# Kernel tuning notes

Measured on AMD Instinct MI355X. Metric: run time of the kernel, lower is better.

The kernel has to match this reference:

```python
import jax, jax.numpy as jnp
import numpy as np
import math

D_MODEL = 1024
NUM_HEADS = 16
D_K = D_MODEL // NUM_HEADS
THETA = 10000.0
B, T = 2, 2048


def _trunc_normal(key, shape, std):
    # truncated normal in [-3std, 3std]
    return jax.random.truncated_normal(key, -3.0, 3.0, shape, jnp.float32) * std


def setup_inputs() -> dict:
    key = jax.random.key(0)
    ks = jax.random.split(key, 6)
    sigma = math.sqrt(2.0 / (D_MODEL + D_MODEL))
    x = jax.random.normal(ks[0], (B, T, D_MODEL), jnp.float32)
    Wq = _trunc_normal(ks[1], (D_MODEL, D_MODEL), sigma)  # [out, in]
    Wk = _trunc_normal(ks[2], (D_MODEL, D_MODEL), sigma)
    Wv = _trunc_normal(ks[3], (D_MODEL, D_MODEL), sigma)
    Wo = _trunc_normal(ks[4], (D_MODEL, D_MODEL), sigma)
    token_positions = jnp.arange(T, dtype=jnp.int64 if jax.config.read('jax_enable_x64') else jnp.int32)
    return {"x": x, "Wq": Wq, "Wk": Wk, "Wv": Wv, "Wo": Wo,
            "token_positions": token_positions}


def _rotate_half(x):
    x0 = x[..., ::2]
    x1 = x[..., 1::2]
    return jnp.stack((-x1, x0), axis=-1).reshape(x.shape)


def _rope(x, token_positions):
    # x: [B, H, T, d_k]; token_positions: [T]
    inv_freq = 1.0 / (THETA ** (jnp.arange(0, D_K, 2, dtype=jnp.float32) / D_K))
    ang = token_positions.astype(jnp.float32)[:, None] * inv_freq  # [T, d_k/2]
    cos = jnp.repeat(jnp.cos(ang), 2, axis=-1)  # [T, d_k]
    sin = jnp.repeat(jnp.sin(ang), 2, axis=-1)
    xdtype = x.dtype
    xf = x.astype(jnp.float32)
    return (xf * cos + _rotate_half(xf) * sin).astype(xdtype)


def reference(x, Wq, Wk, Wv, Wo, token_positions):
    b, t, _ = x.shape

    def proj_split(W):
        h = jnp.einsum('btd,od->bto', x, W)
        return h.reshape(b, t, NUM_HEADS, D_K).transpose(0, 2, 1, 3)  # [B,H,T,d_k]

    Q = _rope(proj_split(Wq), token_positions)
    K = _rope(proj_split(Wk), token_positions)
    V = proj_split(Wv)

    scores = jnp.einsum('bhqd,bhkd->bhqk', Q, K) / math.sqrt(D_K)
    causal = jnp.tril(jnp.ones((t, t), dtype=bool))  # [T,T]
    scores = jnp.where(causal, scores, -jnp.inf)
    weights = jax.nn.softmax(scores, axis=-1)
    attn = jnp.einsum('bhqk,bhkd->bhqd', weights, V)  # [B,H,T,d_v]
    merged = attn.transpose(0, 2, 1, 3).reshape(b, t, D_MODEL)
    return jnp.einsum('btd,od->bto', merged, Wo)
```

## Files before the change

kernel.cpp:

```cpp
#include <hip/hip_runtime.h>
#include <cstdint>
#include <cstddef>

#define DMODEL 1024
#define NHEADS 16
#define DKH    64
#define SEQT   2048
#define NBATCH 2
#define MTOT   (NBATCH*SEQT)

#define QSCALE 0.1803368801111204f

using h16   = _Float16;
using h16x2 = __attribute__((ext_vector_type(2))) h16;
using h16x4 = __attribute__((ext_vector_type(4))) h16;
using h16x8 = __attribute__((ext_vector_type(8))) h16;
using f32x4 = __attribute__((ext_vector_type(4))) float;
using fp16x2_native = __attribute__((ext_vector_type(2))) __fp16;

using as1_void = __attribute__((address_space(1))) void;
using as3_void = __attribute__((address_space(3))) void;

__device__ __forceinline__ void gll16(void* lds, const void* g) {
  __builtin_amdgcn_global_load_lds((const as1_void*)g, (as3_void*)lds, 16, 0, 0);
}

__device__ __forceinline__ h16x2 pkrtz(float a, float b) {
  fp16x2_native t = __builtin_amdgcn_cvt_pkrtz(a, b);
  h16x2 r; r[0] = (h16)t[0]; r[1] = (h16)t[1]; return r;
}

__device__ __forceinline__ h16x4 cvt4(const float4 v) {
  h16x4 o; o[0] = (h16)v.x; o[1] = (h16)v.y; o[2] = (h16)v.z; o[3] = (h16)v.w; return o;
}

__global__ void prep_kernel(const float4* __restrict__ x,
                            const float4* __restrict__ Wq, const float4* __restrict__ Wk,
                            const float4* __restrict__ Wv, const float4* __restrict__ Wo,
                            h16x4* __restrict__ xb,
                            h16x4* __restrict__ wqb, h16x4* __restrict__ wkb,
                            h16x4* __restrict__ wvb, h16x4* __restrict__ wob,
                            float* __restrict__ ctab, float* __restrict__ stab) {
  const int tid  = blockIdx.x * blockDim.x + threadIdx.x;
  const int nthr = gridDim.x * blockDim.x;
  const int NX4 = MTOT * DMODEL / 4;
  const int NW4 = DMODEL * DMODEL / 4;
  for (int i = tid; i < NX4; i += nthr) xb[i] = cvt4(x[i]);
  for (int i = tid; i < NW4; i += nthr) {
    wqb[i] = cvt4(Wq[i]);
    wkb[i] = cvt4(Wk[i]);
    wvb[i] = cvt4(Wv[i]);
    wob[i] = cvt4(Wo[i]);
  }
  for (int i = tid; i < SEQT * 32; i += nthr) {
    const int t = i >> 5, fi = i & 31;
    float inv = __expf(-0.28782313662425575f * (float)fi);
    float ang = (float)t * inv;
    float s, c;
    sincosf(ang, &s, &c);
    ctab[i] = c; stab[i] = s;
  }
}

__device__ __forceinline__ void gemm128_bt(const h16* __restrict__ A, const h16* __restrict__ Bt,
                                           int m0, int n0, h16* Al, h16* Bl, f32x4 acc[4][4]) {
  const int tid  = threadIdx.x;
  const int lane = tid & 63;
  const int wv   = tid >> 6;
  const int wm = (wv >> 1) * 64, wn = (wv & 1) * 64;
  const int lr = lane & 15, lk = (lane >> 4) * 8;
  const int srow = tid >> 2, scol = (tid & 3) * 8;
  const h16* a0 = A  + (size_t)(m0 + srow) * DMODEL + scol;
  const h16* a1 = a0 + (size_t)64 * DMODEL;
  const h16* b0 = Bt + (size_t)(n0 + srow) * DMODEL + scol;
  const h16* b1 = b0 + (size_t)64 * DMODEL;
  h16* alds0 = Al + wv * 512;
  h16* alds1 = Al + 2048 + wv * 512;
  h16* blds0 = Bl + wv * 512;
  h16* blds1 = Bl + 2048 + wv * 512;

  for (int k0 = 0; k0 < DMODEL; k0 += 32) {
    __syncthreads();
    gll16(alds0, a0 + k0);
    gll16(alds1, a1 + k0);
    gll16(blds0, b0 + k0);
    gll16(blds1, b1 + k0);
    __syncthreads();
    h16x8 af[4], bfr[4];
#pragma unroll
    for (int i = 0; i < 4; ++i) {
      af[i]  = *(const h16x8*)(Al + (wm + i * 16 + lr) * 32 + lk);
      bfr[i] = *(const h16x8*)(Bl + (wn + i * 16 + lr) * 32 + lk);
    }
#pragma unroll
    for (int i = 0; i < 4; ++i)
#pragma unroll
      for (int j = 0; j < 4; ++j)
        acc[i][j] = __builtin_amdgcn_mfma_f32_16x16x32_f16(af[i], bfr[j], acc[i][j], 0, 0, 0);
  }
}

__global__ __launch_bounds__(256, 2) void qkv_kernel(
    const h16* __restrict__ xb,
    const h16* __restrict__ wqb, const h16* __restrict__ wkb, const h16* __restrict__ wvb,
    const float* __restrict__ ctab, const float* __restrict__ stab,
    h16* __restrict__ Qb, h16* __restrict__ Kb, h16* __restrict__ Vt) {
  __shared__ h16 Al[128 * 32], Bl[128 * 32];
  const int which = blockIdx.z;
  const h16* W = (which == 0) ? wqb : (which == 1) ? wkb : wvb;
  const int m0 = blockIdx.x * 128, n0 = blockIdx.y * 128;
  f32x4 acc[4][4];
  const f32x4 zero4 = {0.f, 0.f, 0.f, 0.f};
#pragma unroll
  for (int i = 0; i < 4; ++i)
#pragma unroll
    for (int j = 0; j < 4; ++j) acc[i][j] = zero4;

  gemm128_bt(xb, W, m0, n0, Al, Bl, acc);

  const int lane = threadIdx.x & 63, wv = threadIdx.x >> 6;
  const int wm = (wv >> 1) * 64, wn = (wv & 1) * 64;
  const int lr4 = ((lane >> 4) << 2), lc = lane & 15;
  if (which == 2) {
#pragma unroll
    for (int i = 0; i < 4; ++i) {
      const int m = m0 + wm + i * 16 + lr4;
      const int b = m >> 11, t = m & (SEQT - 1);
#pragma unroll
      for (int j = 0; j < 4; ++j) {
        const int n = n0 + wn + j * 16 + lc;
        const int h = n >> 6, d = n & 63;
        h16x4 o4;
#pragma unroll
        for (int r = 0; r < 4; ++r) o4[r] = (h16)acc[i][j][r];
        *(h16x4*)&Vt[((size_t)(b * NHEADS + h) * DKH + d) * SEQT + t] = o4;
      }
    }
  } else {
#pragma unroll
    for (int i = 0; i < 4; ++i) {
#pragma unroll
      for (int j = 0; j < 4; ++j) {
        const int n = n0 + wn + j * 16 + lc;
        const int h = n >> 6, d = n & 63;
#pragma unroll
        for (int r = 0; r < 4; ++r) {
          const int m = m0 + wm + i * 16 + lr4 + r;
          const int b = m >> 11, t = m & (SEQT - 1);
          float v = acc[i][j][r];
          float pv = __shfl_xor(v, 1);
          const int fi = d >> 1;
          float c = ctab[t * 32 + fi], s = stab[t * 32 + fi];
          float res = (d & 1) ? (v * c + pv * s) : (v * c - pv * s);
          if (which == 0) res *= QSCALE;
          h16* dst = (which == 0) ? Qb : Kb;
          dst[((size_t)(b * NHEADS + h) * SEQT + t) * DKH + d] = (h16)res;
        }
      }
    }
  }
}

__global__ __launch_bounds__(256, 4) void attn_kernel(
    const h16* __restrict__ Qb, const h16* __restrict__ Kb,
    const h16* __restrict__ Vt, h16* __restrict__ Mg) {
  __shared__ h16 Kl[128][76];
  __shared__ h16 Vl[64][140];
  const int linear = blockIdx.x + 32 * blockIdx.y;
  const int v   = linear & 7;
  const int p   = linear >> 3;
  const int w   = p >> 5;
  const int c32 = p & 31;
  const int u   = (c32 + w) & 3;
  const int bh  = c32;
  const int qt  = (u == 0) ? v : (u == 1) ? (15 - v) : (u == 2) ? (16 + v) : (31 - v);
  const int b = bh >> 4, h = bh & 15;
  const int tid = threadIdx.x, lane = tid & 63, wv = tid >> 6;
  const int lr = lane & 15, lg = lane >> 4;
  const int q0 = qt * 64;
  const int qbase = q0 + wv * 16;
  const int q = qbase + lr;
  const h16* Qp = Qb + ((size_t)bh * SEQT + qbase) * DKH;
  const h16* Kp = Kb + (size_t)bh * SEQT * DKH;
  const h16* Vp = Vt + (size_t)bh * DKH * SEQT;

  h16x8 qf[2];
#pragma unroll
  for (int kk = 0; kk < 2; ++kk)
    qf[kk] = *(const h16x8*)(Qp + lr * DKH + kk * 32 + lg * 8);

  float mrow = -3.0e38f, lsum = 0.f;
  f32x4 o[4];
  const f32x4 zero4 = {0.f, 0.f, 0.f, 0.f};
#pragma unroll
  for (int di = 0; di < 4; ++di) o[di] = zero4;

  const int sr = tid >> 2, sc = (tid & 3) * 16;
  const int nkt = (qt >> 1) + 1;
  for (int kt = 0; kt < nkt; ++kt) {
    const int k0 = kt * 128;
    __syncthreads();
#pragma unroll
    for (int half = 0; half < 2; ++half) {
      const int r = half * 64 + sr;
      *(uint4*)&Kl[r][sc]     = *(const uint4*)(Kp + (size_t)(k0 + r) * DKH + sc);
      *(uint4*)&Kl[r][sc + 8] = *(const uint4*)(Kp + (size_t)(k0 + r) * DKH + sc + 8);
    }
#pragma unroll
    for (int half = 0; half < 2; ++half) {
      const int c = half * 64 + sc;
      *(uint4*)&Vl[sr][c]     = *(const uint4*)(Vp + (size_t)sr * SEQT + k0 + c);
      *(uint4*)&Vl[sr][c + 8] = *(const uint4*)(Vp + (size_t)sr * SEQT + k0 + c + 8);
    }
    __syncthreads();

    f32x4 s[8];
    __builtin_amdgcn_s_setprio(1);
#pragma unroll
    for (int ni = 0; ni < 8; ++ni) {
      s[ni] = zero4;
#pragma unroll
      for (int kk = 0; kk < 2; ++kk) {
        h16x8 kf = *(const h16x8*)&Kl[ni * 16 + lr][kk * 32 + lg * 8];
        s[ni] = __builtin_amdgcn_mfma_f32_16x16x32_f16(kf, qf[kk], s[ni], 0, 0, 0);
      }
    }
    __builtin_amdgcn_s_setprio(0);

    if (kt == nkt - 1) {
#pragma unroll
      for (int ni = 0; ni < 8; ++ni)
#pragma unroll
        for (int r = 0; r < 4; ++r) {
          const int key = k0 + ni * 16 + lg * 4 + r;
          if (key > q) s[ni][r] = -3.0e38f;
        }
    }

    float mx = s[0][0];
#pragma unroll
    for (int ni = 0; ni < 8; ++ni)
#pragma unroll
      for (int r = 0; r < 4; ++r) mx = fmaxf(mx, s[ni][r]);
    mx = fmaxf(mx, __shfl_xor(mx, 16));
    mx = fmaxf(mx, __shfl_xor(mx, 32));
    if (mx > mrow + 11.0f) {
      const float mnew = fmaxf(mrow, mx);
      const float scl = exp2f(mrow - mnew);
      mrow = mnew;
      lsum *= scl;
#pragma unroll
      for (int di = 0; di < 4; ++di)
#pragma unroll
        for (int r = 0; r < 4; ++r) o[di][r] *= scl;
    }
    float rs = 0.f;
#pragma unroll
    for (int ni = 0; ni < 8; ++ni)
#pragma unroll
      for (int r = 0; r < 4; ++r) {
        float p2 = exp2f(s[ni][r] - mrow);
        s[ni][r] = p2;
        rs += p2;
      }
    rs += __shfl_xor(rs, 16);
    rs += __shfl_xor(rs, 32);
    lsum += rs;

    __builtin_amdgcn_s_setprio(1);
#pragma unroll
    for (int ni = 0; ni < 8; ++ni) {
      h16x2 plo = pkrtz(s[ni][0], s[ni][1]);
      h16x2 phi = pkrtz(s[ni][2], s[ni][3]);
      h16x4 pb; pb[0] = plo[0]; pb[1] = plo[1]; pb[2] = phi[0]; pb[3] = phi[1];
#pragma unroll
      for (int di = 0; di < 4; ++di) {
        h16x4 va = *(const h16x4*)&Vl[di * 16 + lr][ni * 16 + lg * 4];
        o[di] = __builtin_amdgcn_mfma_f32_16x16x16f16(va, pb, o[di], 0, 0, 0);
      }
    }
    __builtin_amdgcn_s_setprio(0);
  }

  __syncthreads();
  const float inv = 1.0f / lsum;
#pragma unroll
  for (int di = 0; di < 4; ++di) {
    h16x2 lo = pkrtz(o[di][0] * inv, o[di][1] * inv);
    h16x2 hi = pkrtz(o[di][2] * inv, o[di][3] * inv);
    h16x4 o4; o4[0] = lo[0]; o4[1] = lo[1]; o4[2] = hi[0]; o4[3] = hi[1];
    *(h16x4*)&Kl[wv * 16 + lr][di * 16 + lg * 4] = o4;
  }
  __syncthreads();
  {
    const int row = tid >> 2, c0 = (tid & 3) * 16;
    h16* dst = Mg + ((size_t)(b * SEQT + q0 + row)) * DMODEL + h * DKH + c0;
    *(uint4*)dst       = *(const uint4*)&Kl[row][c0];
    *(uint4*)(dst + 8) = *(const uint4*)&Kl[row][c0 + 8];
  }
}

__global__ __launch_bounds__(256, 2) void proj_kernel(
    const h16* __restrict__ Mg, const h16* __restrict__ wob, float* __restrict__ out) {
  __shared__ h16 Al[128 * 32], Bl[128 * 32];
  const int m0 = blockIdx.x * 128, n0 = blockIdx.y * 128;
  f32x4 acc[4][4];
  const f32x4 zero4 = {0.f, 0.f, 0.f, 0.f};
#pragma unroll
  for (int i = 0; i < 4; ++i)
#pragma unroll
    for (int j = 0; j < 4; ++j) acc[i][j] = zero4;

  gemm128_bt(Mg, wob, m0, n0, Al, Bl, acc);

  const int lane = threadIdx.x & 63, wv = threadIdx.x >> 6;
  const int wm = (wv >> 1) * 64, wn = (wv & 1) * 64;
  const int lr4 = ((lane >> 4) << 2), lc = lane & 15;
#pragma unroll
  for (int i = 0; i < 4; ++i)
#pragma unroll
    for (int j = 0; j < 4; ++j) {
      const int n = n0 + wn + j * 16 + lc;
#pragma unroll
      for (int r = 0; r < 4; ++r) {
        const int m = m0 + wm + i * 16 + lr4 + r;
        out[(size_t)m * DMODEL + n] = acc[i][j][r];
      }
    }
}

extern "C" void kernel_launch(void* const* d_in, const int* in_sizes, int n_in,
                              void* d_out, int out_size, void* d_ws, size_t ws_size,
                              hipStream_t stream) {
  (void)in_sizes; (void)n_in; (void)out_size; (void)ws_size;
  const float* x  = (const float*)d_in[0];
  const float* Wq = (const float*)d_in[1];
  const float* Wk = (const float*)d_in[2];
  const float* Wv = (const float*)d_in[3];
  const float* Wo = (const float*)d_in[4];
  float* out = (float*)d_out;

  char* w = (char*)d_ws;
  h16* xb  = (h16*)w; w += (size_t)MTOT * DMODEL * 2;
  h16* wqb = (h16*)w; w += (size_t)DMODEL * DMODEL * 2;
  h16* wkb = (h16*)w; w += (size_t)DMODEL * DMODEL * 2;
  h16* wvb = (h16*)w; w += (size_t)DMODEL * DMODEL * 2;
  h16* wob = (h16*)w; w += (size_t)DMODEL * DMODEL * 2;
  h16* Qb  = (h16*)w; w += (size_t)MTOT * DMODEL * 2;
  h16* Kb  = (h16*)w; w += (size_t)MTOT * DMODEL * 2;
  h16* Vt  = (h16*)w; w += (size_t)MTOT * DMODEL * 2;
  h16* Mg  = (h16*)w; w += (size_t)MTOT * DMODEL * 2;
  float* ctab = (float*)w; w += (size_t)SEQT * 32 * 4;
  float* stab = (float*)w; w += (size_t)SEQT * 32 * 4;

  prep_kernel<<<1024, 256, 0, stream>>>((const float4*)x, (const float4*)Wq, (const float4*)Wk,
                                        (const float4*)Wv, (const float4*)Wo,
                                        (h16x4*)xb, (h16x4*)wqb, (h16x4*)wkb, (h16x4*)wvb,
                                        (h16x4*)wob, ctab, stab);
  qkv_kernel<<<dim3(32, 8, 3), 256, 0, stream>>>(xb, wqb, wkb, wvb, ctab, stab, Qb, Kb, Vt);
  attn_kernel<<<dim3(32, 32), 256, 0, stream>>>(Qb, Kb, Vt, Mg);
  proj_kernel<<<dim3(32, 8), 256, 0, stream>>>(Mg, wob, out);
}
```

Baseline: 115.4 us.

## Prefetch next K/V tiles into registers to overlap global loads with MFMA

The attention loop now issues global loads for the next K tile before the QK^T MFMAs and for the next V tile after them, keeping the data in registers. Each tile is written to LDS only after a barrier shows the current tile is no longer being read. This hides global-memory latency behind compute within a single LDS buffer. The cost is extra registers (eight uint4 per thread), which may lower occupancy, plus an additional barrier per iteration.

```diff
diff --git a/kernel.cpp b/kernel.cpp
--- a/kernel.cpp
+++ b/kernel.cpp
@@ -196,23 +196,46 @@
   for (int di = 0; di < 4; ++di) o[di] = zero4;
 
   const int sr = tid >> 2, sc = (tid & 3) * 16;
+  uint4 ka0, ka1, ka2, ka3;
+  uint4 va0, va1, va2, va3;
+
+#define KISSUE(k0_) {                                                      \
+    const h16* kb_ = Kp + (size_t)(k0_) * DKH;                             \
+    ka0 = *(const uint4*)(kb_ + (size_t)sr * DKH + sc);                    \
+    ka1 = *(const uint4*)(kb_ + (size_t)sr * DKH + sc + 8);                \
+    ka2 = *(const uint4*)(kb_ + (size_t)(64 + sr) * DKH + sc);             \
+    ka3 = *(const uint4*)(kb_ + (size_t)(64 + sr) * DKH + sc + 8);         \
+  }
+#define KWRITE() {                                                         \
+    *(uint4*)&Kl[sr][sc]          = ka0;                                   \
+    *(uint4*)&Kl[sr][sc + 8]      = ka1;                                   \
+    *(uint4*)&Kl[64 + sr][sc]     = ka2;                                   \
+    *(uint4*)&Kl[64 + sr][sc + 8] = ka3;                                   \
+  }
+#define VISSUE(k0_) {                                                      \
+    const h16* vb_ = Vp + (k0_);                                           \
+    va0 = *(const uint4*)(vb_ + (size_t)sr * SEQT + sc);                   \
+    va1 = *(const uint4*)(vb_ + (size_t)sr * SEQT + sc + 8);               \
+    va2 = *(const uint4*)(vb_ + (size_t)sr * SEQT + 64 + sc);              \
+    va3 = *(const uint4*)(vb_ + (size_t)sr * SEQT + 64 + sc + 8);          \
+  }
+#define VWRITE() {                                                         \
+    *(uint4*)&Vl[sr][sc]          = va0;                                   \
+    *(uint4*)&Vl[sr][sc + 8]      = va1;                                   \
+    *(uint4*)&Vl[sr][64 + sc]     = va2;                                   \
+    *(uint4*)&Vl[sr][64 + sc + 8] = va3;                                   \
+  }
+
+  KISSUE(0); VISSUE(0);
+  KWRITE(); VWRITE();
+  __syncthreads();
+
   const int nkt = (qt >> 1) + 1;
   for (int kt = 0; kt < nkt; ++kt) {
     const int k0 = kt * 128;
-    __syncthreads();
-#pragma unroll
-    for (int half = 0; half < 2; ++half) {
-      const int r = half * 64 + sr;
-      *(uint4*)&Kl[r][sc]     = *(const uint4*)(Kp + (size_t)(k0 + r) * DKH + sc);
-      *(uint4*)&Kl[r][sc + 8] = *(const uint4*)(Kp + (size_t)(k0 + r) * DKH + sc + 8);
-    }
-#pragma unroll
-    for (int half = 0; half < 2; ++half) {
-      const int c = half * 64 + sc;
-      *(uint4*)&Vl[sr][c]     = *(const uint4*)(Vp + (size_t)sr * SEQT + k0 + c);
-      *(uint4*)&Vl[sr][c + 8] = *(const uint4*)(Vp + (size_t)sr * SEQT + k0 + c + 8);
-    }
-    __syncthreads();
+    const bool more = (kt + 1 < nkt);
+
+    if (more) { KISSUE(k0 + 128); __builtin_amdgcn_sched_barrier(0); }
 
     f32x4 s[8];
     __builtin_amdgcn_s_setprio(1);
@@ -226,6 +249,12 @@
       }
     }
     __builtin_amdgcn_s_setprio(0);
+
+    __syncthreads();
+    if (more) {
+      KWRITE();
+      VISSUE(k0 + 128); __builtin_amdgcn_sched_barrier(0);
+    }
 
     if (kt == nkt - 1) {
 #pragma unroll
@@ -280,7 +309,14 @@
       }
     }
     __builtin_amdgcn_s_setprio(0);
-  }
+
+    __syncthreads();
+    if (more) VWRITE();
+  }
+#undef KISSUE
+#undef KWRITE
+#undef VISSUE
+#undef VWRITE
 
   __syncthreads();
   const float inv = 1.0f / lsum;
```

New measurement: 117.5 us. Within noise of the previous version (+1.8%).
